# Kernel tuning notes

Measured on AMD Instinct MI355X. Metric: run time of the kernel, lower is better.

Reference implementation:

```python
import jax, jax.numpy as jnp
import numpy as np

EMBED_DIM = 1024
N_HEAD = 16

def setup_inputs() -> dict:
    key = jax.random.key(0)
    ks = jax.random.split(key, 5)
    C = EMBED_DIM
    x = jax.random.normal(ks[0], (2, 2048, C), dtype=jnp.float32)
    s = 1.0 / np.sqrt(C)
    W_attn = jax.random.normal(ks[1], (C, 3 * C), dtype=jnp.float32) * s
    b_attn = jnp.zeros((3 * C,), dtype=jnp.float32)
    W_proj = jax.random.normal(ks[2], (C, C), dtype=jnp.float32) * s
    b_proj = jnp.zeros((C,), dtype=jnp.float32)
    return {"x": x, "W_attn": W_attn, "b_attn": b_attn, "W_proj": W_proj, "b_proj": b_proj}

def reference(x, W_attn, b_attn, W_proj, b_proj):
    B, T, C = x.shape
    H = N_HEAD
    D = C // H
    qkv = x @ W_attn + b_attn                      # [B,T,3C]
    q, k, v = jnp.split(qkv, 3, axis=-1)
    # [B,H,T,D]
    q = q.reshape(B, T, H, D).transpose(0, 2, 1, 3)
    k = k.reshape(B, T, H, D).transpose(0, 2, 1, 3)
    v = v.reshape(B, T, H, D).transpose(0, 2, 1, 3)
    att = jnp.einsum('bhqd,bhkd->bhqk', q, k) * (1.0 / jnp.sqrt(jnp.asarray(D, x.dtype)))
    causal = jnp.tril(jnp.ones((T, T), dtype=bool))
    att = jnp.where(causal, att, -jnp.inf)
    att = jax.nn.softmax(att, axis=-1)
    y = jnp.einsum('bhqk,bhkd->bhqd', att, v)      # [B,H,T,D]
    y = y.transpose(0, 2, 1, 3).reshape(B, T, C)
    return y @ W_proj + b_proj
```

## Files before the change

kernel.cpp:

```cpp
#include <hip/hip_runtime.h>
#include <stdint.h>

typedef __attribute__((ext_vector_type(4))) float f32x4;
typedef __attribute__((ext_vector_type(8))) __bf16 bf16x8;
typedef __attribute__((ext_vector_type(8))) unsigned short u16x8;

__device__ __forceinline__ unsigned short f2b(float f) {
  unsigned u = __float_as_uint(f);
  u += 0x7FFFu + ((u >> 16) & 1u);
  return (unsigned short)(u >> 16);
}
__device__ __forceinline__ float b2f(unsigned short s) {
  unsigned u = (unsigned)s << 16;
  return __uint_as_float(u);
}
__device__ __forceinline__ unsigned cvtpk_bf16(float lo, float hi) {
  unsigned r;
  asm("v_cvt_pk_bf16_f32 %0, %1, %2" : "=v"(r) : "v"(lo), "v"(hi));
  return r;
}

__device__ __forceinline__ void gload_lds16(const void* g, void* l) {
  typedef __attribute__((address_space(1))) void GV1;
  typedef __attribute__((address_space(3))) void LV3;
  __builtin_amdgcn_global_load_lds((GV1*)(void*)g, (LV3*)l, 16, 0, 0);
}

__global__ __launch_bounds__(256) void convert_f32_bf16(const float* __restrict__ in,
                                                        unsigned short* __restrict__ out, int n) {
  int i = (blockIdx.x * 256 + threadIdx.x) * 8;
  if (i >= n) return;
  float4 a = *(const float4*)(in + i);
  float4 b = *(const float4*)(in + i + 4);
  u16x8 r;
  r[0] = f2b(a.x); r[1] = f2b(a.y); r[2] = f2b(a.z); r[3] = f2b(a.w);
  r[4] = f2b(b.x); r[5] = f2b(b.y); r[6] = f2b(b.z); r[7] = f2b(b.w);
  *(u16x8*)(out + i) = r;
}

__global__ __launch_bounds__(256) void transpose_f32_bf16(const float* __restrict__ W,
                                                          unsigned short* __restrict__ Wt,
                                                          int K, int N) {
  __shared__ unsigned short tile[32][33];
  int n0 = blockIdx.x * 32, k0 = blockIdx.y * 32;
  int tx = threadIdx.x, ty = threadIdx.y;
  #pragma unroll
  for (int j = 0; j < 32; j += 8)
    tile[ty + j][tx] = f2b(W[(size_t)(k0 + ty + j) * N + n0 + tx]);
  __syncthreads();
  #pragma unroll
  for (int j = 0; j < 32; j += 8)
    Wt[(size_t)(n0 + ty + j) * K + k0 + tx] = tile[tx][ty + j];
}

template <bool OUT_BF16>
__global__ __launch_bounds__(256) void gemm_bt(const unsigned short* __restrict__ A,
                                               const unsigned short* __restrict__ Bt,
                                               const float* __restrict__ bias,
                                               void* __restrict__ Cout,
                                               int M, int N, int K) {
  __shared__ unsigned short As[128 * 64];
  __shared__ unsigned short Bs[128 * 64];
  const int m0 = blockIdx.x * 128, n0 = blockIdx.y * 128;
  const int tid = threadIdx.x;
  const int w = tid >> 6, l = tid & 63;
  const int wm = w >> 1, wn = w & 1;
  const int c = l & 15, g = l >> 4;
  f32x4 acc[4][4] = {};
  for (int k0 = 0; k0 < K; k0 += 64) {
    #pragma unroll
    for (int i = 0; i < 4; ++i) {
      int rb = w * 32 + i * 8;
      gload_lds16(A + (size_t)(m0 + rb + (l >> 3)) * K + k0 + (l & 7) * 8, &As[rb * 64]);
      gload_lds16(Bt + (size_t)(n0 + rb + (l >> 3)) * K + k0 + (l & 7) * 8, &Bs[rb * 64]);
    }
    __syncthreads();
    #pragma unroll
    for (int ks = 0; ks < 2; ++ks) {
      bf16x8 af[4], bf[4];
      #pragma unroll
      for (int mi = 0; mi < 4; ++mi)
        af[mi] = *(const bf16x8*)&As[(wm * 64 + mi * 16 + c) * 64 + ks * 32 + g * 8];
      #pragma unroll
      for (int ni = 0; ni < 4; ++ni)
        bf[ni] = *(const bf16x8*)&Bs[(wn * 64 + ni * 16 + c) * 64 + ks * 32 + g * 8];
      #pragma unroll
      for (int mi = 0; mi < 4; ++mi)
        #pragma unroll
        for (int ni = 0; ni < 4; ++ni)
          acc[mi][ni] = __builtin_amdgcn_mfma_f32_16x16x32_bf16(af[mi], bf[ni], acc[mi][ni], 0, 0, 0);
    }
    __syncthreads();
  }
  #pragma unroll
  for (int mi = 0; mi < 4; ++mi) {
    #pragma unroll
    for (int ni = 0; ni < 4; ++ni) {
      int colg = n0 + wn * 64 + ni * 16 + c;
      float bv = bias[colg];
      #pragma unroll
      for (int r = 0; r < 4; ++r) {
        int rowg = m0 + wm * 64 + mi * 16 + 4 * g + r;
        float v = acc[mi][ni][r] + bv;
        if (OUT_BF16)
          ((unsigned short*)Cout)[(size_t)rowg * N + colg] = f2b(v);
        else
          ((float*)Cout)[(size_t)rowg * N + colg] = v;
      }
    }
  }
}

__global__ __launch_bounds__(256) void attn_kernel(const unsigned short* __restrict__ qkv,
                                                   unsigned short* __restrict__ partO,
                                                   float* __restrict__ partML) {
  __shared__ unsigned short K_lds[2][64 * 64];
  __shared__ unsigned short V_lds[2][64 * 64];
  const int bid = blockIdx.x;
  const int bh = bid & 31;
  const int cid = bid >> 5;
  int qt, ct;
  if (cid < 32)      { qt = cid;      ct = 0; }
  else if (cid < 56) { qt = cid - 24; ct = 1; }
  else if (cid < 72) { qt = cid - 40; ct = 2; }
  else               { qt = cid - 48; ct = 3; }
  const int t0 = ct * 8;
  const int ntl = min(qt + 1 - t0, 8);
  const bool hasdiag = (t0 + ntl - 1) == qt;
  const int b = bh >> 4, h = bh & 15;
  const int tid = threadIdx.x, w = tid >> 6, l = tid & 63;
  const int c = l & 15, g = l >> 4;
  const int hi = g >> 1;
  const int srcA = c + ((g & 1) << 5);
  const int srcB = srcA + 16;
  const size_t row0 = (size_t)b * 2048;
  const int vp = tid & 31, vcb = tid >> 5;
  const float SCL = 0.18033688f;

  const int q0w = qt * 64 + w * 16;
  const int qg = q0w + c;

  bf16x8 qf[2];
  #pragma unroll
  for (int ks = 0; ks < 2; ++ks)
    qf[ks] = *(const bf16x8*)(qkv + (row0 + qg) * 3072 + h * 64 + ks * 32 + g * 8);

  f32x4 acc[4] = {};
  float mstate = -1e30f, lstate = 0.f;

  {
    #pragma unroll
    for (int i = 0; i < 2; ++i) {
      int rb = w * 16 + i * 8;
      int row = rb + (l >> 3);
      int ch = (l & 7) ^ (row & 7);
      gload_lds16(qkv + (row0 + t0 * 64 + row) * 3072 + 1024 + h * 64 + ch * 8,
                  &K_lds[0][rb * 64]);
    }
    size_t tr = row0 + t0 * 64 + 2 * vp;
    u16x8 v0 = *(const u16x8*)(qkv + tr * 3072 + 2048 + h * 64 + vcb * 8);
    u16x8 v1 = *(const u16x8*)(qkv + (tr + 1) * 3072 + 2048 + h * 64 + vcb * 8);
    char* Vb = (char*)V_lds[0];
    #pragma unroll
    for (int jj = 0; jj < 8; ++jj) {
      int d = vcb * 8 + jj;
      int off = d * 128 + ((4 * vp) ^ ((d & 7) << 4));
      *(unsigned int*)(Vb + off) = (unsigned int)v0[jj] | ((unsigned int)v1[jj] << 16);
    }
  }
  __syncthreads();

  for (int lt = 0; lt < ntl; ++lt) {
    const int cur = lt & 1;
    const int kv0 = (t0 + lt) * 64;
    const bool pre = (lt + 1 < ntl);
    u16x8 v0n, v1n;
    if (pre) {
      const int kvn = kv0 + 64;
      #pragma unroll
      for (int ii = 0; ii < 2; ++ii) {
        int rb = w * 16 + ii * 8;
        int row = rb + (l >> 3);
        int ch = (l & 7) ^ (row & 7);
        gload_lds16(qkv + (row0 + kvn + row) * 3072 + 1024 + h * 64 + ch * 8,
                    &K_lds[cur ^ 1][rb * 64]);
      }
      size_t tr = row0 + kvn + 2 * vp;
      v0n = *(const u16x8*)(qkv + tr * 3072 + 2048 + h * 64 + vcb * 8);
      v1n = *(const u16x8*)(qkv + (tr + 1) * 3072 + 2048 + h * 64 + vcb * 8);
    }
    const char* Kb = (const char*)K_lds[cur];
    const char* Vb = (const char*)V_lds[cur];
    f32x4 s[4] = {};
    #pragma unroll
    for (int ks = 0; ks < 2; ++ks) {
      bf16x8 kf[4];
      #pragma unroll
      for (int nk = 0; nk < 4; ++nk) {
        int row = nk * 16 + c;
        kf[nk] = *(const bf16x8*)(Kb + row * 128 + ((ks * 64 + g * 16) ^ ((row & 7) << 4)));
      }
      __builtin_amdgcn_s_setprio(1);
      #pragma unroll
      for (int nk = 0; nk < 4; ++nk)
        s[nk] = __builtin_amdgcn_mfma_f32_16x16x32_bf16(kf[nk], qf[ks], s[nk], 0, 0, 0);
      __builtin_amdgcn_s_setprio(0);
    }
    if (hasdiag && lt == ntl - 1) {
      #pragma unroll
      for (int nk = 0; nk < 4; ++nk)
        #pragma unroll
        for (int r = 0; r < 4; ++r) {
          int kvg = kv0 + nk * 16 + 4 * g + r;
          if (kvg > qg) s[nk][r] = -1e30f;
        }
    }
    float a0 = fmaxf(fmaxf(s[0][0], s[0][1]), fmaxf(s[0][2], s[0][3]));
    float a1 = fmaxf(fmaxf(s[1][0], s[1][1]), fmaxf(s[1][2], s[1][3]));
    float a2 = fmaxf(fmaxf(s[2][0], s[2][1]), fmaxf(s[2][2], s[2][3]));
    float a3 = fmaxf(fmaxf(s[3][0], s[3][1]), fmaxf(s[3][2], s[3][3]));
    float mx = fmaxf(fmaxf(a0, a1), fmaxf(a2, a3));
    mx = fmaxf(mx, __shfl_xor(mx, 16));
    mx = fmaxf(mx, __shfl_xor(mx, 32));
    if (!__all(mx <= mstate)) {
      float mnew = fmaxf(mstate, mx);
      float alpha = exp2f((mstate - mnew) * SCL);
      mstate = mnew;
      lstate *= alpha;
      #pragma unroll
      for (int nd = 0; nd < 4; ++nd) acc[nd] *= alpha;
    }
    float ms = mstate * SCL;
    #pragma unroll
    for (int nk = 0; nk < 4; ++nk) {
      #pragma unroll
      for (int r = 0; r < 4; ++r) s[nk][r] = exp2f(fmaf(s[nk][r], SCL, -ms));
      lstate += (s[nk][0] + s[nk][1]) + (s[nk][2] + s[nk][3]);
    }
    unsigned pk[4][2];
    #pragma unroll
    for (int nk = 0; nk < 4; ++nk) {
      pk[nk][0] = cvtpk_bf16(s[nk][0], s[nk][1]);
      pk[nk][1] = cvtpk_bf16(s[nk][2], s[nk][3]);
    }
    #pragma unroll
    for (int vks = 0; vks < 2; ++vks) {
      unsigned rA00 = __shfl(pk[2 * vks][0], srcA, 64);
      unsigned rA01 = __shfl(pk[2 * vks][1], srcA, 64);
      unsigned rA10 = __shfl(pk[2 * vks + 1][0], srcA, 64);
      unsigned rA11 = __shfl(pk[2 * vks + 1][1], srcA, 64);
      unsigned rB00 = __shfl(pk[2 * vks][0], srcB, 64);
      unsigned rB01 = __shfl(pk[2 * vks][1], srcB, 64);
      unsigned rB10 = __shfl(pk[2 * vks + 1][0], srcB, 64);
      unsigned rB11 = __shfl(pk[2 * vks + 1][1], srcB, 64);
      union { unsigned u[4]; bf16x8 v; } pa;
      pa.u[0] = hi ? rA10 : rA00;
      pa.u[1] = hi ? rA11 : rA01;
      pa.u[2] = hi ? rB10 : rB00;
      pa.u[3] = hi ? rB11 : rB01;
      bf16x8 vf[4];
      #pragma unroll
      for (int nd = 0; nd < 4; ++nd) {
        int row = nd * 16 + c;
        vf[nd] = *(const bf16x8*)(Vb + row * 128 + ((vks * 64 + g * 16) ^ ((row & 7) << 4)));
      }
      __builtin_amdgcn_s_setprio(1);
      #pragma unroll
      for (int nd = 0; nd < 4; ++nd)
        acc[nd] = __builtin_amdgcn_mfma_f32_16x16x32_bf16(vf[nd], pa.v, acc[nd], 0, 0, 0);
      __builtin_amdgcn_s_setprio(0);
    }
    if (pre) {
      char* Vbn = (char*)V_lds[cur ^ 1];
      #pragma unroll
      for (int jj = 0; jj < 8; ++jj) {
        int d = vcb * 8 + jj;
        int off = d * 128 + ((4 * vp) ^ ((d & 7) << 4));
        *(unsigned int*)(Vbn + off) = (unsigned int)v0n[jj] | ((unsigned int)v1n[jj] << 16);
      }
    }
    __syncthreads();
  }

  float lsum = lstate;
  lsum += __shfl_xor(lsum, 16);
  lsum += __shfl_xor(lsum, 32);
  const int qrow = w * 16 + c;
  #pragma unroll
  for (int nd = 0; nd < 4; ++nd) {
    ushort4 o4;
    o4.x = f2b(acc[nd][0]); o4.y = f2b(acc[nd][1]);
    o4.z = f2b(acc[nd][2]); o4.w = f2b(acc[nd][3]);
    *(ushort4*)(partO + (size_t)bid * 4096 + qrow * 64 + nd * 16 + 4 * g) = o4;
  }
  if (g == 0) {
    partML[(size_t)bid * 128 + qrow * 2 + 0] = mstate;
    partML[(size_t)bid * 128 + qrow * 2 + 1] = lsum;
  }
}

__global__ __launch_bounds__(256) void attn_combine(const unsigned short* __restrict__ partO,
                                                    const float* __restrict__ partML,
                                                    unsigned short* __restrict__ out) {
  const int bid = blockIdx.x;
  const int qt = bid >> 5, bh = bid & 31;
  const int b = bh >> 4, h = bh & 15;
  const int np = (qt >> 3) + 1;
  const int t = threadIdx.x;
  const int row = t >> 2, cg = (t & 3) * 16;
  const float SCL = 0.18033688f;
  int slot0 = ((qt +  0) << 5) | bh;
  int slot1 = ((qt + 24) << 5) | bh;
  int slot2 = ((qt + 40) << 5) | bh;
  int slot3 = ((qt + 48) << 5) | bh;
  float mstar = partML[(size_t)slot0 * 128 + row * 2];
  if (np > 1) mstar = fmaxf(mstar, partML[(size_t)slot1 * 128 + row * 2]);
  if (np > 2) mstar = fmaxf(mstar, partML[(size_t)slot2 * 128 + row * 2]);
  if (np > 3) mstar = fmaxf(mstar, partML[(size_t)slot3 * 128 + row * 2]);
  float L = 0.f;
  float o[16];
  #pragma unroll
  for (int j = 0; j < 16; ++j) o[j] = 0.f;
  #pragma unroll
  for (int p = 0; p < 4; ++p) {
    if (p < np) {
      int slot = p == 0 ? slot0 : (p == 1 ? slot1 : (p == 2 ? slot2 : slot3));
      float mp = partML[(size_t)slot * 128 + row * 2 + 0];
      float lp = partML[(size_t)slot * 128 + row * 2 + 1];
      float wgt = exp2f((mp - mstar) * SCL);
      L = fmaf(wgt, lp, L);
      const unsigned short* src = partO + (size_t)slot * 4096 + row * 64 + cg;
      u16x8 a = *(const u16x8*)src;
      u16x8 bb = *(const u16x8*)(src + 8);
      #pragma unroll
      for (int j = 0; j < 8; ++j) {
        o[j]     = fmaf(b2f(a[j]),  wgt, o[j]);
        o[j + 8] = fmaf(b2f(bb[j]), wgt, o[j + 8]);
      }
    }
  }
  float rinv = 1.0f / L;
  u16x8 r0, r1;
  #pragma unroll
  for (int j = 0; j < 8; ++j) {
    r0[j] = f2b(o[j] * rinv);
    r1[j] = f2b(o[j + 8] * rinv);
  }
  size_t trow = (size_t)b * 2048 + qt * 64 + row;
  *(u16x8*)(out + trow * 1024 + h * 64 + cg) = r0;
  *(u16x8*)(out + trow * 1024 + h * 64 + cg + 8) = r1;
}

extern "C" void kernel_launch(void* const* d_in, const int* in_sizes, int n_in,
                              void* d_out, int out_size, void* d_ws, size_t ws_size,
                              hipStream_t stream) {
  const float* x      = (const float*)d_in[0];
  const float* W_attn = (const float*)d_in[1];
  const float* b_attn = (const float*)d_in[2];
  const float* W_proj = (const float*)d_in[3];
  const float* b_proj = (const float*)d_in[4];
  float* out = (float*)d_out;

  char* ws = (char*)d_ws;
  unsigned short* Wproj_t  = (unsigned short*)(ws + 0);
  unsigned short* qkv      = (unsigned short*)(ws + 2097152);
  unsigned short* x_bf     = (unsigned short*)(ws + 27262976);
  unsigned short* Wattn_t  = (unsigned short*)(ws + 35651584);
  unsigned short* partO    = (unsigned short*)(ws + 27262976);
  unsigned short* attn_out = (unsigned short*)(ws + 48234496);
  float*          partML   = (float*)(ws + 56623104);

  convert_f32_bf16<<<2048, 256, 0, stream>>>(x, x_bf, 4194304);
  transpose_f32_bf16<<<dim3(96, 32), dim3(32, 8), 0, stream>>>(W_attn, Wattn_t, 1024, 3072);
  transpose_f32_bf16<<<dim3(32, 32), dim3(32, 8), 0, stream>>>(W_proj, Wproj_t, 1024, 1024);

  gemm_bt<true><<<dim3(32, 24), 256, 0, stream>>>(x_bf, Wattn_t, b_attn, qkv, 4096, 3072, 1024);
  attn_kernel<<<2560, 256, 0, stream>>>(qkv, partO, partML);
  attn_combine<<<1024, 256, 0, stream>>>(partO, partML, attn_out);
  gemm_bt<false><<<dim3(32, 8), 256, 0, stream>>>(attn_out, Wproj_t, b_proj, out, 4096, 1024, 1024);
}
```

Measured before the change: 153.1 us.

## Use 128-row query tiles with 8-wave blocks sharing each KV tile

The attention kernel now processes 128 query rows per block with 512 threads (8 waves), so every K/V tile staged in LDS is reused by twice as many query rows. Each thread loads half as much per tile. The split-KV chunk mapping and the combine kernel are rewritten for the new tile count. Waves whose query rows lie entirely above a KV tile skip the compute through a per-wave causal check, which adds imbalance inside the block and halves the block count.

After: 232.6 us. +51.9%, slower.

```diff
diff --git a/kernel.cpp b/kernel.cpp
--- a/kernel.cpp
+++ b/kernel.cpp
@@ -4,6 +4,7 @@
 typedef __attribute__((ext_vector_type(4))) float f32x4;
 typedef __attribute__((ext_vector_type(8))) __bf16 bf16x8;
 typedef __attribute__((ext_vector_type(8))) unsigned short u16x8;
+typedef __attribute__((ext_vector_type(4))) unsigned short u16x4;
 
 __device__ __forceinline__ unsigned short f2b(float f) {
   unsigned u = __float_as_uint(f);
@@ -111,22 +112,22 @@
   }
 }
 
-__global__ __launch_bounds__(256) void attn_kernel(const unsigned short* __restrict__ qkv,
-                                                   unsigned short* __restrict__ partO,
-                                                   float* __restrict__ partML) {
+__global__ __launch_bounds__(512, 8) void attn_kernel(const unsigned short* __restrict__ qkv,
+                                                      unsigned short* __restrict__ partO,
+                                                      float* __restrict__ partML) {
   __shared__ unsigned short K_lds[2][64 * 64];
   __shared__ unsigned short V_lds[2][64 * 64];
   const int bid = blockIdx.x;
   const int bh = bid & 31;
   const int cid = bid >> 5;
   int qt, ct;
-  if (cid < 32)      { qt = cid;      ct = 0; }
-  else if (cid < 56) { qt = cid - 24; ct = 1; }
-  else if (cid < 72) { qt = cid - 40; ct = 2; }
-  else               { qt = cid - 48; ct = 3; }
+  if (cid < 4)       { qt = cid;            ct = 0; }
+  else if (cid < 12) { int e = cid - 4;  qt = 4 + (e >> 1);  ct = e & 1; }
+  else if (cid < 24) { int e = cid - 12; int q3 = e / 3; qt = 8 + q3; ct = e - 3 * q3; }
+  else               { int e = cid - 24; qt = 12 + (e >> 2); ct = e & 3; }
+  const int ntt = 2 * qt + 2;
   const int t0 = ct * 8;
-  const int ntl = min(qt + 1 - t0, 8);
-  const bool hasdiag = (t0 + ntl - 1) == qt;
+  const int ntl = min(ntt - t0, 8);
   const int b = bh >> 4, h = bh & 15;
   const int tid = threadIdx.x, w = tid >> 6, l = tid & 63;
   const int c = l & 15, g = l >> 4;
@@ -137,7 +138,7 @@
   const int vp = tid & 31, vcb = tid >> 5;
   const float SCL = 0.18033688f;
 
-  const int q0w = qt * 64 + w * 16;
+  const int q0w = qt * 128 + w * 16;
   const int qg = q0w + c;
 
   bf16x8 qf[2];
@@ -149,21 +150,18 @@
   float mstate = -1e30f, lstate = 0.f;
 
   {
-    #pragma unroll
-    for (int i = 0; i < 2; ++i) {
-      int rb = w * 16 + i * 8;
-      int row = rb + (l >> 3);
-      int ch = (l & 7) ^ (row & 7);
-      gload_lds16(qkv + (row0 + t0 * 64 + row) * 3072 + 1024 + h * 64 + ch * 8,
-                  &K_lds[0][rb * 64]);
-    }
+    int rb = w * 8;
+    int row = rb + (l >> 3);
+    int ch = (l & 7) ^ (row & 7);
+    gload_lds16(qkv + (row0 + t0 * 64 + row) * 3072 + 1024 + h * 64 + ch * 8,
+                &K_lds[0][rb * 64]);
     size_t tr = row0 + t0 * 64 + 2 * vp;
-    u16x8 v0 = *(const u16x8*)(qkv + tr * 3072 + 2048 + h * 64 + vcb * 8);
-    u16x8 v1 = *(const u16x8*)(qkv + (tr + 1) * 3072 + 2048 + h * 64 + vcb * 8);
+    u16x4 v0 = *(const u16x4*)(qkv + tr * 3072 + 2048 + h * 64 + vcb * 4);
+    u16x4 v1 = *(const u16x4*)(qkv + (tr + 1) * 3072 + 2048 + h * 64 + vcb * 4);
     char* Vb = (char*)V_lds[0];
     #pragma unroll
-    for (int jj = 0; jj < 8; ++jj) {
-      int d = vcb * 8 + jj;
+    for (int jj = 0; jj < 4; ++jj) {
+      int d = vcb * 4 + jj;
       int off = d * 128 + ((4 * vp) ^ ((d & 7) << 4));
       *(unsigned int*)(Vb + off) = (unsigned int)v0[jj] | ((unsigned int)v1[jj] << 16);
     }
@@ -174,107 +172,106 @@
     const int cur = lt & 1;
     const int kv0 = (t0 + lt) * 64;
     const bool pre = (lt + 1 < ntl);
-    u16x8 v0n, v1n;
+    u16x4 v0n, v1n;
     if (pre) {
       const int kvn = kv0 + 64;
-      #pragma unroll
-      for (int ii = 0; ii < 2; ++ii) {
-        int rb = w * 16 + ii * 8;
-        int row = rb + (l >> 3);
-        int ch = (l & 7) ^ (row & 7);
-        gload_lds16(qkv + (row0 + kvn + row) * 3072 + 1024 + h * 64 + ch * 8,
-                    &K_lds[cur ^ 1][rb * 64]);
-      }
+      int rb = w * 8;
+      int row = rb + (l >> 3);
+      int ch = (l & 7) ^ (row & 7);
+      gload_lds16(qkv + (row0 + kvn + row) * 3072 + 1024 + h * 64 + ch * 8,
+                  &K_lds[cur ^ 1][rb * 64]);
       size_t tr = row0 + kvn + 2 * vp;
-      v0n = *(const u16x8*)(qkv + tr * 3072 + 2048 + h * 64 + vcb * 8);
-      v1n = *(const u16x8*)(qkv + (tr + 1) * 3072 + 2048 + h * 64 + vcb * 8);
-    }
-    const char* Kb = (const char*)K_lds[cur];
-    const char* Vb = (const char*)V_lds[cur];
-    f32x4 s[4] = {};
-    #pragma unroll
-    for (int ks = 0; ks < 2; ++ks) {
-      bf16x8 kf[4];
+      v0n = *(const u16x4*)(qkv + tr * 3072 + 2048 + h * 64 + vcb * 4);
+      v1n = *(const u16x4*)(qkv + (tr + 1) * 3072 + 2048 + h * 64 + vcb * 4);
+    }
+    if (kv0 <= q0w + 15) {
+      const char* Kb = (const char*)K_lds[cur];
+      const char* Vb = (const char*)V_lds[cur];
+      f32x4 s[4] = {};
+      #pragma unroll
+      for (int ks = 0; ks < 2; ++ks) {
+        bf16x8 kf[4];
+        #pragma unroll
+        for (int nk = 0; nk < 4; ++nk) {
+          int row = nk * 16 + c;
+          kf[nk] = *(const bf16x8*)(Kb + row * 128 + ((ks * 64 + g * 16) ^ ((row & 7) << 4)));
+        }
+        __builtin_amdgcn_s_setprio(1);
+        #pragma unroll
+        for (int nk = 0; nk < 4; ++nk)
+          s[nk] = __builtin_amdgcn_mfma_f32_16x16x32_bf16(kf[nk], qf[ks], s[nk], 0, 0, 0);
+        __builtin_amdgcn_s_setprio(0);
+      }
+      if (kv0 + 63 > q0w) {
+        #pragma unroll
+        for (int nk = 0; nk < 4; ++nk)
+          #pragma unroll
+          for (int r = 0; r < 4; ++r) {
+            int kvg = kv0 + nk * 16 + 4 * g + r;
+            if (kvg > qg) s[nk][r] = -1e30f;
+          }
+      }
+      float a0 = fmaxf(fmaxf(s[0][0], s[0][1]), fmaxf(s[0][2], s[0][3]));
+      float a1 = fmaxf(fmaxf(s[1][0], s[1][1]), fmaxf(s[1][2], s[1][3]));
+      float a2 = fmaxf(fmaxf(s[2][0], s[2][1]), fmaxf(s[2][2], s[2][3]));
+      float a3 = fmaxf(fmaxf(s[3][0], s[3][1]), fmaxf(s[3][2], s[3][3]));
+      float mx = fmaxf(fmaxf(a0, a1), fmaxf(a2, a3));
+      mx = fmaxf(mx, __shfl_xor(mx, 16));
+      mx = fmaxf(mx, __shfl_xor(mx, 32));
+      if (!__all(mx <= mstate)) {
+        float mnew = fmaxf(mstate, mx);
+        float alpha = exp2f((mstate - mnew) * SCL);
+        mstate = mnew;
+        lstate *= alpha;
+        #pragma unroll
+        for (int nd = 0; nd < 4; ++nd) acc[nd] *= alpha;
+      }
+      float ms = mstate * SCL;
       #pragma unroll
       for (int nk = 0; nk < 4; ++nk) {
-        int row = nk * 16 + c;
-        kf[nk] = *(const bf16x8*)(Kb + row * 128 + ((ks * 64 + g * 16) ^ ((row & 7) << 4)));
-      }
-      __builtin_amdgcn_s_setprio(1);
-      #pragma unroll
-      for (int nk = 0; nk < 4; ++nk)
-        s[nk] = __builtin_amdgcn_mfma_f32_16x16x32_bf16(kf[nk], qf[ks], s[nk], 0, 0, 0);
-      __builtin_amdgcn_s_setprio(0);
-    }
-    if (hasdiag && lt == ntl - 1) {
-      #pragma unroll
-      for (int nk = 0; nk < 4; ++nk)
-        #pragma unroll
-        for (int r = 0; r < 4; ++r) {
-          int kvg = kv0 + nk * 16 + 4 * g + r;
-          if (kvg > qg) s[nk][r] = -1e30f;
+        #pragma unroll
+        for (int r = 0; r < 4; ++r) s[nk][r] = exp2f(fmaf(s[nk][r], SCL, -ms));
+        lstate += (s[nk][0] + s[nk][1]) + (s[nk][2] + s[nk][3]);
+      }
+      unsigned pk[4][2];
+      #pragma unroll
+      for (int nk = 0; nk < 4; ++nk) {
+        pk[nk][0] = cvtpk_bf16(s[nk][0], s[nk][1]);
+        pk[nk][1] = cvtpk_bf16(s[nk][2], s[nk][3]);
+      }
+      #pragma unroll
+      for (int vks = 0; vks < 2; ++vks) {
+        unsigned rA00 = __shfl(pk[2 * vks][0], srcA, 64);
+        unsigned rA01 = __shfl(pk[2 * vks][1], srcA, 64);
+        unsigned rA10 = __shfl(pk[2 * vks + 1][0], srcA, 64);
+        unsigned rA11 = __shfl(pk[2 * vks + 1][1], srcA, 64);
+        unsigned rB00 = __shfl(pk[2 * vks][0], srcB, 64);
+        unsigned rB01 = __shfl(pk[2 * vks][1], srcB, 64);
+        unsigned rB10 = __shfl(pk[2 * vks + 1][0], srcB, 64);
+        unsigned rB11 = __shfl(pk[2 * vks + 1][1], srcB, 64);
+        union { unsigned u[4]; bf16x8 v; } pa;
+        pa.u[0] = hi ? rA10 : rA00;
+        pa.u[1] = hi ? rA11 : rA01;
+        pa.u[2] = hi ? rB10 : rB00;
+        pa.u[3] = hi ? rB11 : rB01;
+        bf16x8 vf[4];
+        #pragma unroll
+        for (int nd = 0; nd < 4; ++nd) {
+          int row = nd * 16 + c;
+          vf[nd] = *(const bf16x8*)(Vb + row * 128 + ((vks * 64 + g * 16) ^ ((row & 7) << 4)));
         }
-    }
-    float a0 = fmaxf(fmaxf(s[0][0], s[0][1]), fmaxf(s[0][2], s[0][3]));
-    float a1 = fmaxf(fmaxf(s[1][0], s[1][1]), fmaxf(s[1][2], s[1][3]));
-    float a2 = fmaxf(fmaxf(s[2][0], s[2][1]), fmaxf(s[2][2], s[2][3]));
-    float a3 = fmaxf(fmaxf(s[3][0], s[3][1]), fmaxf(s[3][2], s[3][3]));
-    float mx = fmaxf(fmaxf(a0, a1), fmaxf(a2, a3));
-    mx = fmaxf(mx, __shfl_xor(mx, 16));
-    mx = fmaxf(mx, __shfl_xor(mx, 32));
-    if (!__all(mx <= mstate)) {
-      float mnew = fmaxf(mstate, mx);
-      float alpha = exp2f((mstate - mnew) * SCL);
-      mstate = mnew;
-      lstate *= alpha;
-      #pragma unroll
-      for (int nd = 0; nd < 4; ++nd) acc[nd] *= alpha;
-    }
-    float ms = mstate * SCL;
-    #pragma unroll
-    for (int nk = 0; nk < 4; ++nk) {
-      #pragma unroll
-      for (int r = 0; r < 4; ++r) s[nk][r] = exp2f(fmaf(s[nk][r], SCL, -ms));
-      lstate += (s[nk][0] + s[nk][1]) + (s[nk][2] + s[nk][3]);
-    }
-    unsigned pk[4][2];
-    #pragma unroll
-    for (int nk = 0; nk < 4; ++nk) {
-      pk[nk][0] = cvtpk_bf16(s[nk][0], s[nk][1]);
-      pk[nk][1] = cvtpk_bf16(s[nk][2], s[nk][3]);
-    }
-    #pragma unroll
-    for (int vks = 0; vks < 2; ++vks) {
-      unsigned rA00 = __shfl(pk[2 * vks][0], srcA, 64);
-      unsigned rA01 = __shfl(pk[2 * vks][1], srcA, 64);
-      unsigned rA10 = __shfl(pk[2 * vks + 1][0], srcA, 64);
-      unsigned rA11 = __shfl(pk[2 * vks + 1][1], srcA, 64);
-      unsigned rB00 = __shfl(pk[2 * vks][0], srcB, 64);
-      unsigned rB01 = __shfl(pk[2 * vks][1], srcB, 64);
-      unsigned rB10 = __shfl(pk[2 * vks + 1][0], srcB, 64);
-      unsigned rB11 = __shfl(pk[2 * vks + 1][1], srcB, 64);
-      union { unsigned u[4]; bf16x8 v; } pa;
-      pa.u[0] = hi ? rA10 : rA00;
-      pa.u[1] = hi ? rA11 : rA01;
-      pa.u[2] = hi ? rB10 : rB00;
-      pa.u[3] = hi ? rB11 : rB01;
-      bf16x8 vf[4];
-      #pragma unroll
-      for (int nd = 0; nd < 4; ++nd) {
-        int row = nd * 16 + c;
-        vf[nd] = *(const bf16x8*)(Vb + row * 128 + ((vks * 64 + g * 16) ^ ((row & 7) << 4)));
-      }
-      __builtin_amdgcn_s_setprio(1);
-      #pragma unroll
-      for (int nd = 0; nd < 4; ++nd)
-        acc[nd] = __builtin_amdgcn_mfma_f32_16x16x32_bf16(vf[nd], pa.v, acc[nd], 0, 0, 0);
-      __builtin_amdgcn_s_setprio(0);
+        __builtin_amdgcn_s_setprio(1);
+        #pragma unroll
+        for (int nd = 0; nd < 4; ++nd)
+          acc[nd] = __builtin_amdgcn_mfma_f32_16x16x32_bf16(vf[nd], pa.v, acc[nd], 0, 0, 0);
+        __builtin_amdgcn_s_setprio(0);
+      }
     }
     if (pre) {
       char* Vbn = (char*)V_lds[cur ^ 1];
       #pragma unroll
-      for (int jj = 0; jj < 8; ++jj) {
-        int d = vcb * 8 + jj;
+      for (int jj = 0; jj < 4; ++jj) {
+        int d = vcb * 4 + jj;
         int off = d * 128 + ((4 * vp) ^ ((d & 7) << 4));
         *(unsigned int*)(Vbn + off) = (unsigned int)v0n[jj] | ((unsigned int)v1n[jj] << 16);
       }
@@ -291,11 +288,11 @@
     ushort4 o4;
     o4.x = f2b(acc[nd][0]); o4.y = f2b(acc[nd][1]);
     o4.z = f2b(acc[nd][2]); o4.w = f2b(acc[nd][3]);
-    *(ushort4*)(partO + (size_t)bid * 4096 + qrow * 64 + nd * 16 + 4 * g) = o4;
+    *(ushort4*)(partO + (size_t)bid * 8192 + qrow * 64 + nd * 16 + 4 * g) = o4;
   }
   if (g == 0) {
-    partML[(size_t)bid * 128 + qrow * 2 + 0] = mstate;
-    partML[(size_t)bid * 128 + qrow * 2 + 1] = lsum;
+    partML[(size_t)bid * 256 + qrow * 2 + 0] = mstate;
+    partML[(size_t)bid * 256 + qrow * 2 + 1] = lsum;
   }
 }
 
@@ -305,50 +302,50 @@
   const int bid = blockIdx.x;
   const int qt = bid >> 5, bh = bid & 31;
   const int b = bh >> 4, h = bh & 15;
-  const int np = (qt >> 3) + 1;
+  const int np = (2 * qt + 9) >> 3;
+  const int base = (qt < 4) ? qt
+                 : (qt < 8) ? 4 + 2 * (qt - 4)
+                 : (qt < 12) ? 12 + 3 * (qt - 8)
+                 : 24 + 4 * (qt - 12);
   const int t = threadIdx.x;
-  const int row = t >> 2, cg = (t & 3) * 16;
+  const int row = t >> 1, cg = (t & 1) * 32;
   const float SCL = 0.18033688f;
-  int slot0 = ((qt +  0) << 5) | bh;
-  int slot1 = ((qt + 24) << 5) | bh;
-  int slot2 = ((qt + 40) << 5) | bh;
-  int slot3 = ((qt + 48) << 5) | bh;
-  float mstar = partML[(size_t)slot0 * 128 + row * 2];
-  if (np > 1) mstar = fmaxf(mstar, partML[(size_t)slot1 * 128 + row * 2]);
-  if (np > 2) mstar = fmaxf(mstar, partML[(size_t)slot2 * 128 + row * 2]);
-  if (np > 3) mstar = fmaxf(mstar, partML[(size_t)slot3 * 128 + row * 2]);
+  float mstar = -1e30f;
+  #pragma unroll
+  for (int p = 0; p < 4; ++p)
+    if (p < np)
+      mstar = fmaxf(mstar, partML[(size_t)(((base + p) << 5) | bh) * 256 + row * 2]);
   float L = 0.f;
-  float o[16];
-  #pragma unroll
-  for (int j = 0; j < 16; ++j) o[j] = 0.f;
+  float o[32];
+  #pragma unroll
+  for (int j = 0; j < 32; ++j) o[j] = 0.f;
   #pragma unroll
   for (int p = 0; p < 4; ++p) {
     if (p < np) {
-      int slot = p == 0 ? slot0 : (p == 1 ? slot1 : (p == 2 ? slot2 : slot3));
-      float mp = partML[(size_t)slot * 128 + row * 2 + 0];
-      float lp = partML[(size_t)slot * 128 + row * 2 + 1];
+      int slot = ((base + p) << 5) | bh;
+      float mp = partML[(size_t)slot * 256 + row * 2 + 0];
+      float lp = partML[(size_t)slot * 256 + row * 2 + 1];
       float wgt = exp2f((mp - mstar) * SCL);
       L = fmaf(wgt, lp, L);
-      const unsigned short* src = partO + (size_t)slot * 4096 + row * 64 + cg;
-      u16x8 a = *(const u16x8*)src;
-      u16x8 bb = *(const u16x8*)(src + 8);
-      #pragma unroll
-      for (int j = 0; j < 8; ++j) {
-        o[j]     = fmaf(b2f(a[j]),  wgt, o[j]);
-        o[j + 8] = fmaf(b2f(bb[j]), wgt, o[j + 8]);
+      const unsigned short* src = partO + (size_t)slot * 8192 + row * 64 + cg;
+      #pragma unroll
+      for (int q = 0; q < 4; ++q) {
+        u16x8 a = *(const u16x8*)(src + q * 8);
+        #pragma unroll
+        for (int j = 0; j < 8; ++j)
+          o[q * 8 + j] = fmaf(b2f(a[j]), wgt, o[q * 8 + j]);
       }
     }
   }
   float rinv = 1.0f / L;
-  u16x8 r0, r1;
-  #pragma unroll
-  for (int j = 0; j < 8; ++j) {
-    r0[j] = f2b(o[j] * rinv);
-    r1[j] = f2b(o[j + 8] * rinv);
-  }
-  size_t trow = (size_t)b * 2048 + qt * 64 + row;
-  *(u16x8*)(out + trow * 1024 + h * 64 + cg) = r0;
-  *(u16x8*)(out + trow * 1024 + h * 64 + cg + 8) = r1;
+  size_t trow = (size_t)b * 2048 + qt * 128 + row;
+  #pragma unroll
+  for (int q = 0; q < 4; ++q) {
+    u16x8 r;
+    #pragma unroll
+    for (int j = 0; j < 8; ++j) r[j] = f2b(o[q * 8 + j] * rinv);
+    *(u16x8*)(out + trow * 1024 + h * 64 + cg + q * 8) = r;
+  }
 }
 
 extern "C" void kernel_launch(void* const* d_in, const int* in_sizes, int n_in,
@@ -375,7 +372,7 @@
   transpose_f32_bf16<<<dim3(32, 32), dim3(32, 8), 0, stream>>>(W_proj, Wproj_t, 1024, 1024);
 
   gemm_bt<true><<<dim3(32, 24), 256, 0, stream>>>(x_bf, Wattn_t, b_attn, qkv, 4096, 3072, 1024);
-  attn_kernel<<<2560, 256, 0, stream>>>(qkv, partO, partML);
-  attn_combine<<<1024, 256, 0, stream>>>(partO, partML, attn_out);
+  attn_kernel<<<1280, 512, 0, stream>>>(qkv, partO, partML);
+  attn_combine<<<512, 256, 0, stream>>>(partO, partML, attn_out);
   gemm_bt<false><<<dim3(32, 8), 256, 0, stream>>>(attn_out, Wproj_t, b_proj, out, 4096, 1024, 1024);
 }
```
